# Kernel optimization log

Hardware: AMD Instinct MI355X
Metric: run time of the kernel (lower is better)

## Reference

```python
import jax, jax.numpy as jnp
import numpy as np

N_NODES = 100000
N_EDGES = 1600000
NFEAT, NHID, NCLASS = 64, 128, 32


def _glorot(key, shape):
    fan_in, fan_out = shape[0], shape[1]
    lim = np.sqrt(6.0 / (fan_in + fan_out))
    return jax.random.uniform(key, shape, jnp.float32, -lim, lim)


def setup_inputs() -> dict:
    key = jax.random.key(0)
    ks = jax.random.split(key, 12)
    x = jax.random.normal(ks[0], (N_NODES, NFEAT), jnp.float32)
    edge_idx = jax.random.randint(ks[1], (2, N_EDGES), 0, N_NODES, jnp.int64)
    edge_weight = jax.random.uniform(ks[2], (N_EDGES,), jnp.float32)
    return {
        "x": x,
        "edge_idx": edge_idx,
        "edge_weight": edge_weight,
        # SAGEConv 1: out = mean_agg(x) @ Wl1 + b1 + x @ Wr1
        "Wl1": _glorot(ks[3], (NFEAT, NHID)),
        "Wr1": _glorot(ks[4], (NFEAT, NHID)),
        "b1": jnp.zeros((NHID,), jnp.float32),
        # SAGEConv 2
        "Wl2": _glorot(ks[5], (NHID, NHID)),
        "Wr2": _glorot(ks[6], (NHID, NHID)),
        "b2": jnp.zeros((NHID,), jnp.float32),
        # fc head: Linear(nhid, nclass) -> Linear(nclass, 1)
        "Wfc1": _glorot(ks[7], (NHID, NCLASS)),
        "bfc1": jnp.zeros((NCLASS,), jnp.float32),
        "Wfc2": _glorot(ks[8], (NCLASS, 1)),
        "bfc2": jnp.zeros((1,), jnp.float32),
    }


def _sage_conv(x, src, dst, Wl, Wr, b, n_nodes):
    # mean aggregation of source features at destination nodes
    msg_sum = jax.ops.segment_sum(x[src], dst, num_segments=n_nodes)  # [N, d]
    deg = jax.ops.segment_sum(jnp.ones((src.shape[0], 1), x.dtype), dst,
                              num_segments=n_nodes)                    # [N, 1]
    mean = msg_sum / jnp.maximum(deg, 1.0)
    return mean @ Wl + b + x @ Wr


def reference(x, edge_idx, edge_weight, Wl1, Wr1, b1, Wl2, Wr2, b2,
              Wfc1, bfc1, Wfc2, bfc2):
    n_nodes = x.shape[0]
    src, dst = edge_idx[0], edge_idx[1]
    # dropout is identity in eval mode (training=False)
    h = _sage_conv(x, src, dst, Wl1, Wr1, b1, n_nodes)   # [N, nhid]
    h = _sage_conv(h, src, dst, Wl2, Wr2, b2, n_nodes)   # [N, nhid]
    h = h @ Wfc1 + bfc1                                   # [N, nclass]
    out = h @ Wfc2 + bfc2                                 # [N, 1]
    return out
```

## Files before the change

kernel.cpp:

```cpp
#include <hip/hip_runtime.h>

#define S_SHIFT 8
#define S_NODES 256
#define NBKT    400
#define CAP     5120
#define CHUNK   8192
#define NREP    4
#define FTH     512
#define NDOTS   160

__global__ __launch_bounds__(FTH) void fused_kernel(
    const float* __restrict__ x,
    const int* __restrict__ src, const int* __restrict__ dst,
    int E, int N, int B, int nscat,
    int* __restrict__ cursor, unsigned* __restrict__ bucket,
    const float* __restrict__ Wl1, const float* __restrict__ Wr1, const float* __restrict__ b1,
    const float* __restrict__ Wl2, const float* __restrict__ Wr2, const float* __restrict__ b2,
    const float* __restrict__ Wfc1, const float* __restrict__ bfc1,
    const float* __restrict__ Wfc2, const float* __restrict__ bfc2,
    float* __restrict__ ga, float2* __restrict__ gbc, float* __restrict__ c01)
{
    __shared__ int hist[NBKT], lbase[NBKT], lcur[NBKT];
    __shared__ float wv[192], uu[128], vl2[128], vr2[128], w2[32];
    int t = threadIdx.x;
    int l = t & 63;
    int w = t >> 6;

    if ((int)blockIdx.x < nscat) {
        int e0 = blockIdx.x * CHUNK;
        int cnt = E - e0; if (cnt > CHUNK) cnt = CHUNK;
        for (int i = t; i < B; i += FTH) hist[i] = 0;
        __syncthreads();
        for (int i = t; i < cnt; i += FTH)
            atomicAdd(&hist[dst[e0 + i] >> S_SHIFT], 1);
        __syncthreads();
        for (int i = t; i < B; i += FTH) {
            lcur[i] = 0;
            if (hist[i] > 0) lbase[i] = atomicAdd(&cursor[i], hist[i]);
        }
        __syncthreads();
        for (int i = t; i < cnt; i += FTH) {
            int d = dst[e0 + i], s = src[e0 + i];
            int bb = d >> S_SHIFT;
            int off = atomicAdd(&lcur[bb], 1);
            bucket[(size_t)bb * CAP + (unsigned)(lbase[bb] + off)] =
                ((unsigned)s << S_SHIFT) | (unsigned)(d & (S_NODES - 1));
        }
    } else {
        if (t < 32) w2[t] = Wfc2[t];
        __syncthreads();
        for (int j = 0; j < 16; ++j) {
            int i = w + 8 * j;
            float p = (l < 32) ? Wfc1[i * 32 + l] * w2[l] : 0.f;
            for (int m = 16; m; m >>= 1) p += __shfl_xor(p, m);
            if (l == 0) uu[i] = p;
        }
        __syncthreads();
        for (int j = 0; j < 16; ++j) {
            int i = w + 8 * j;
            float ua = uu[l], ub = uu[64 + l];
            float pa = Wl2[i * 128 + l] * ua + Wl2[i * 128 + 64 + l] * ub;
            float pb = Wr2[i * 128 + l] * ua + Wr2[i * 128 + 64 + l] * ub;
            for (int m = 32; m; m >>= 1) { pa += __shfl_xor(pa, m); pb += __shfl_xor(pb, m); }
            if (l == 0) { vl2[i] = pa; vr2[i] = pb; }
        }
        __syncthreads();
        for (int j = 0; j < 8; ++j) {
            int i = w + 8 * j;
            float l1a = Wl1[i * 128 + l], l1b = Wl1[i * 128 + 64 + l];
            float r1a = Wr1[i * 128 + l], r1b = Wr1[i * 128 + 64 + l];
            float La = vl2[l], Lb = vl2[64 + l], Ra = vr2[l], Rb = vr2[64 + l];
            float pc = l1a * La + l1b * Lb;
            float pb = l1a * Ra + l1b * Rb + r1a * La + r1b * Lb;
            float pa = r1a * Ra + r1b * Rb;
            for (int m = 32; m; m >>= 1) {
                pa += __shfl_xor(pa, m); pb += __shfl_xor(pb, m); pc += __shfl_xor(pc, m);
            }
            if (l == 0) { wv[i] = pa; wv[64 + i] = pb; wv[128 + i] = pc; }
        }
        if ((int)blockIdx.x == nscat && w == 7) {
            float p0 = b1[l] * vr2[l] + b1[64 + l] * vr2[64 + l]
                     + b2[l] * uu[l] + b2[64 + l] * uu[64 + l];
            if (l < 32) p0 += bfc1[l] * w2[l];
            float p1 = b1[l] * vl2[l] + b1[64 + l] * vl2[64 + l];
            for (int m = 32; m; m >>= 1) { p0 += __shfl_xor(p0, m); p1 += __shfl_xor(p1, m); }
            if (l == 0) { c01[0] = p0 + bfc2[0]; c01[1] = p1; }
        }
        __syncthreads();

        int fp = l & 15, sub = l >> 4;
        float4 wa4 = ((const float4*)wv)[fp];
        float4 wb4 = ((const float4*)wv)[16 + fp];
        float4 wc4 = ((const float4*)wv)[32 + fp];
        const float4* x4 = (const float4*)x;
        int Q = (N + 3) >> 2;
        for (int qd = ((int)blockIdx.x - nscat) * 8 + w; qd < Q; qd += NDOTS * 8) {
            int node = qd * 4 + sub;
            float a = 0.f, b = 0.f, c = 0.f;
            if (node < N) {
                float4 v = x4[(size_t)node * 16 + fp];
                a = v.x * wa4.x + v.y * wa4.y + v.z * wa4.z + v.w * wa4.w;
                b = v.x * wb4.x + v.y * wb4.y + v.z * wb4.z + v.w * wb4.w;
                c = v.x * wc4.x + v.y * wc4.y + v.z * wc4.z + v.w * wc4.w;
            }
            for (int m = 8; m; m >>= 1) {
                a += __shfl_xor(a, m); b += __shfl_xor(b, m); c += __shfl_xor(c, m);
            }
            if (fp == 0 && node < N) { ga[node] = a; gbc[node] = make_float2(b, c); }
        }
    }
}

__global__ __launch_bounds__(512) void aggA_kernel(
    const unsigned* __restrict__ bucket, const int* __restrict__ cursor,
    const float2* __restrict__ gbc, const float* __restrict__ ga,
    const float* __restrict__ c01,
    float* __restrict__ q, float* __restrict__ t1, float* __restrict__ inv, int N)
{
    __shared__ float aB[NREP][S_NODES], aC[NREP][S_NODES];
    __shared__ int cnt[NREP][S_NODES];
    int t = threadIdx.x, b = blockIdx.x;
    int r = (t >> 6) & (NREP - 1);
    float* aBf = (float*)aB; float* aCf = (float*)aC; int* cnf = (int*)cnt;
    for (int i = t; i < NREP * S_NODES; i += 512) { aBf[i] = 0.f; aCf[i] = 0.f; cnf[i] = 0; }
    __syncthreads();
    int n = cursor[b];
    const unsigned* bp = bucket + (size_t)b * CAP;
    for (int i = t; i < n; i += 512) {
        unsigned uu = bp[i];
        float2 g = gbc[uu >> S_SHIFT];
        int dl = uu & (S_NODES - 1);
        atomicAdd(&aB[r][dl], g.x);
        atomicAdd(&aC[r][dl], g.y);
        atomicAdd(&cnt[r][dl], 1);
    }
    __syncthreads();
    if (t < S_NODES) {
        int node = (b << S_SHIFT) + t;
        if (node < N) {
            float sb = aB[0][t] + aB[1][t] + aB[2][t] + aB[3][t];
            float sc = aC[0][t] + aC[1][t] + aC[2][t] + aC[3][t];
            int d = cnt[0][t] + cnt[1][t] + cnt[2][t] + cnt[3][t];
            float iv = 1.0f / ((d > 0) ? (float)d : 1.0f);
            inv[node] = iv;
            q[node]   = iv * sc;
            t1[node]  = ga[node] + iv * sb + c01[0] + (d > 0 ? c01[1] : 0.f);
        }
    }
}

__global__ __launch_bounds__(512) void aggB_kernel(
    const unsigned* __restrict__ bucket, const int* __restrict__ cursor,
    const float* __restrict__ q, const float* __restrict__ t1,
    const float* __restrict__ inv, float* __restrict__ out, int N)
{
    __shared__ float a2[NREP][S_NODES];
    int t = threadIdx.x, b = blockIdx.x;
    int r = (t >> 6) & (NREP - 1);
    float* a2f = (float*)a2;
    for (int i = t; i < NREP * S_NODES; i += 512) a2f[i] = 0.f;
    __syncthreads();
    int n = cursor[b];
    const unsigned* bp = bucket + (size_t)b * CAP;
    for (int i = t; i < n; i += 512) {
        unsigned uu = bp[i];
        atomicAdd(&a2[r][uu & (S_NODES - 1)], q[uu >> S_SHIFT]);
    }
    __syncthreads();
    if (t < S_NODES) {
        int node = (b << S_SHIFT) + t;
        if (node < N)
            out[node] = t1[node] + inv[node] * (a2[0][t] + a2[1][t] + a2[2][t] + a2[3][t]);
    }
}

extern "C" void kernel_launch(void* const* d_in, const int* in_sizes, int n_in,
                              void* d_out, int out_size, void* d_ws, size_t ws_size,
                              hipStream_t stream) {
    const float* x    = (const float*)d_in[0];
    const int*   eidx = (const int*)d_in[1];
    const float* Wl1  = (const float*)d_in[3];
    const float* Wr1  = (const float*)d_in[4];
    const float* b1   = (const float*)d_in[5];
    const float* Wl2  = (const float*)d_in[6];
    const float* Wr2  = (const float*)d_in[7];
    const float* b2   = (const float*)d_in[8];
    const float* Wfc1 = (const float*)d_in[9];
    const float* bfc1 = (const float*)d_in[10];
    const float* Wfc2 = (const float*)d_in[11];
    const float* bfc2 = (const float*)d_in[12];

    const int N = in_sizes[0] / 64;
    const int E = in_sizes[2];
    const int* src = eidx;
    const int* dst = eidx + E;
    const int B = (N + S_NODES - 1) / S_NODES;
    const int nscat = (E + CHUNK - 1) / CHUNK;

    char* ws = (char*)d_ws;
    int*      cursor = (int*)(ws);
    float*    c01    = (float*)(ws + 2048);
    float*    ga     = (float*)(ws + 4096);
    float*    q      = (float*)(ws + 4096 + (size_t)N * 4);
    float*    t1     = (float*)(ws + 4096 + (size_t)N * 8);
    float*    inv    = (float*)(ws + 4096 + (size_t)N * 12);
    float2*   gbc    = (float2*)(ws + 4096 + (size_t)N * 16);
    unsigned* bucket = (unsigned*)(ws + 4096 + (size_t)N * 24);

    hipMemsetAsync(cursor, 0, 2048, stream);

    fused_kernel<<<nscat + NDOTS, FTH, 0, stream>>>(
        x, src, dst, E, N, B, nscat, cursor, bucket,
        Wl1, Wr1, b1, Wl2, Wr2, b2, Wfc1, bfc1, Wfc2, bfc2,
        ga, gbc, c01);

    aggA_kernel<<<B, 512, 0, stream>>>(bucket, cursor, gbc, ga, c01, q, t1, inv, N);
    aggB_kernel<<<B, 512, 0, stream>>>(bucket, cursor, q, t1, inv, (float*)d_out, N);
}
```

Measured before the change: 171.1 us.

## Merge scatter and dot-product roles into uniform blocks with register-cached edges

The prep kernel no longer splits its blocks into edge-scatter blocks and node dot-product blocks. Every block now folds the weight matrices, scatters a smaller chunk of edges, then handles a grid-strided share of the per-node dot products. Edge src/dst values are loaded once into registers and reused between the histogram pass and the scatter pass, so they are not read from global memory twice. In exchange, every block repeats the small weight-folding work, and the halved chunk size means more global cursor atomics and more blocks.

```diff
diff --git a/kernel.cpp b/kernel.cpp
--- a/kernel.cpp
+++ b/kernel.cpp
@@ -4,15 +4,14 @@
 #define S_NODES 256
 #define NBKT    400
 #define CAP     5120
-#define CHUNK   8192
+#define CHUNK   4096
+#define EPT     8
 #define NREP    4
-#define FTH     512
-#define NDOTS   160
-
-__global__ __launch_bounds__(FTH) void fused_kernel(
+
+__global__ __launch_bounds__(512) void prep_kernel(
     const float* __restrict__ x,
     const int* __restrict__ src, const int* __restrict__ dst,
-    int E, int N, int B, int nscat,
+    int E, int N, int B,
     int* __restrict__ cursor, unsigned* __restrict__ bucket,
     const float* __restrict__ Wl1, const float* __restrict__ Wr1, const float* __restrict__ b1,
     const float* __restrict__ Wl2, const float* __restrict__ Wr2, const float* __restrict__ b2,
@@ -26,75 +25,86 @@
     int l = t & 63;
     int w = t >> 6;
 
-    if ((int)blockIdx.x < nscat) {
+    if (t < 32) w2[t] = Wfc2[t];
+    __syncthreads();
+    for (int j = 0; j < 16; ++j) {
+        int i = w + 8 * j;
+        float p = (l < 32) ? Wfc1[i * 32 + l] * w2[l] : 0.f;
+        for (int m = 16; m; m >>= 1) p += __shfl_xor(p, m);
+        if (l == 0) uu[i] = p;
+    }
+    __syncthreads();
+    for (int j = 0; j < 16; ++j) {
+        int i = w + 8 * j;
+        float ua = uu[l], ub = uu[64 + l];
+        float pa = Wl2[i * 128 + l] * ua + Wl2[i * 128 + 64 + l] * ub;
+        float pb = Wr2[i * 128 + l] * ua + Wr2[i * 128 + 64 + l] * ub;
+        for (int m = 32; m; m >>= 1) { pa += __shfl_xor(pa, m); pb += __shfl_xor(pb, m); }
+        if (l == 0) { vl2[i] = pa; vr2[i] = pb; }
+    }
+    __syncthreads();
+    for (int j = 0; j < 8; ++j) {
+        int i = w + 8 * j;
+        float l1a = Wl1[i * 128 + l], l1b = Wl1[i * 128 + 64 + l];
+        float r1a = Wr1[i * 128 + l], r1b = Wr1[i * 128 + 64 + l];
+        float La = vl2[l], Lb = vl2[64 + l], Ra = vr2[l], Rb = vr2[64 + l];
+        float pc = l1a * La + l1b * Lb;
+        float pb = l1a * Ra + l1b * Rb + r1a * La + r1b * Lb;
+        float pa = r1a * Ra + r1b * Rb;
+        for (int m = 32; m; m >>= 1) {
+            pa += __shfl_xor(pa, m); pb += __shfl_xor(pb, m); pc += __shfl_xor(pc, m);
+        }
+        if (l == 0) { wv[i] = pa; wv[64 + i] = pb; wv[128 + i] = pc; }
+    }
+    if (blockIdx.x == 0 && w == 7) {
+        float p0 = b1[l] * vr2[l] + b1[64 + l] * vr2[64 + l]
+                 + b2[l] * uu[l] + b2[64 + l] * uu[64 + l];
+        if (l < 32) p0 += bfc1[l] * w2[l];
+        float p1 = b1[l] * vl2[l] + b1[64 + l] * vl2[64 + l];
+        for (int m = 32; m; m >>= 1) { p0 += __shfl_xor(p0, m); p1 += __shfl_xor(p1, m); }
+        if (l == 0) { c01[0] = p0 + bfc2[0]; c01[1] = p1; }
+    }
+
+    {
         int e0 = blockIdx.x * CHUNK;
         int cnt = E - e0; if (cnt > CHUNK) cnt = CHUNK;
-        for (int i = t; i < B; i += FTH) hist[i] = 0;
+        int sd[EPT], ss[EPT];
+        for (int i = t; i < B; i += 512) hist[i] = 0;
         __syncthreads();
-        for (int i = t; i < cnt; i += FTH)
-            atomicAdd(&hist[dst[e0 + i] >> S_SHIFT], 1);
+        for (int k = 0; k < EPT; ++k) {
+            int i = t + k * 512;
+            if (i < cnt) {
+                sd[k] = dst[e0 + i];
+                ss[k] = src[e0 + i];
+                atomicAdd(&hist[sd[k] >> S_SHIFT], 1);
+            }
+        }
         __syncthreads();
-        for (int i = t; i < B; i += FTH) {
+        for (int i = t; i < B; i += 512) {
             lcur[i] = 0;
             if (hist[i] > 0) lbase[i] = atomicAdd(&cursor[i], hist[i]);
         }
         __syncthreads();
-        for (int i = t; i < cnt; i += FTH) {
-            int d = dst[e0 + i], s = src[e0 + i];
-            int bb = d >> S_SHIFT;
-            int off = atomicAdd(&lcur[bb], 1);
-            bucket[(size_t)bb * CAP + (unsigned)(lbase[bb] + off)] =
-                ((unsigned)s << S_SHIFT) | (unsigned)(d & (S_NODES - 1));
-        }
-    } else {
-        if (t < 32) w2[t] = Wfc2[t];
-        __syncthreads();
-        for (int j = 0; j < 16; ++j) {
-            int i = w + 8 * j;
-            float p = (l < 32) ? Wfc1[i * 32 + l] * w2[l] : 0.f;
-            for (int m = 16; m; m >>= 1) p += __shfl_xor(p, m);
-            if (l == 0) uu[i] = p;
-        }
-        __syncthreads();
-        for (int j = 0; j < 16; ++j) {
-            int i = w + 8 * j;
-            float ua = uu[l], ub = uu[64 + l];
-            float pa = Wl2[i * 128 + l] * ua + Wl2[i * 128 + 64 + l] * ub;
-            float pb = Wr2[i * 128 + l] * ua + Wr2[i * 128 + 64 + l] * ub;
-            for (int m = 32; m; m >>= 1) { pa += __shfl_xor(pa, m); pb += __shfl_xor(pb, m); }
-            if (l == 0) { vl2[i] = pa; vr2[i] = pb; }
-        }
-        __syncthreads();
-        for (int j = 0; j < 8; ++j) {
-            int i = w + 8 * j;
-            float l1a = Wl1[i * 128 + l], l1b = Wl1[i * 128 + 64 + l];
-            float r1a = Wr1[i * 128 + l], r1b = Wr1[i * 128 + 64 + l];
-            float La = vl2[l], Lb = vl2[64 + l], Ra = vr2[l], Rb = vr2[64 + l];
-            float pc = l1a * La + l1b * Lb;
-            float pb = l1a * Ra + l1b * Rb + r1a * La + r1b * Lb;
-            float pa = r1a * Ra + r1b * Rb;
-            for (int m = 32; m; m >>= 1) {
-                pa += __shfl_xor(pa, m); pb += __shfl_xor(pb, m); pc += __shfl_xor(pc, m);
-            }
-            if (l == 0) { wv[i] = pa; wv[64 + i] = pb; wv[128 + i] = pc; }
-        }
-        if ((int)blockIdx.x == nscat && w == 7) {
-            float p0 = b1[l] * vr2[l] + b1[64 + l] * vr2[64 + l]
-                     + b2[l] * uu[l] + b2[64 + l] * uu[64 + l];
-            if (l < 32) p0 += bfc1[l] * w2[l];
-            float p1 = b1[l] * vl2[l] + b1[64 + l] * vl2[64 + l];
-            for (int m = 32; m; m >>= 1) { p0 += __shfl_xor(p0, m); p1 += __shfl_xor(p1, m); }
-            if (l == 0) { c01[0] = p0 + bfc2[0]; c01[1] = p1; }
-        }
-        __syncthreads();
-
+        for (int k = 0; k < EPT; ++k) {
+            int i = t + k * 512;
+            if (i < cnt) {
+                int bb = sd[k] >> S_SHIFT;
+                int off = atomicAdd(&lcur[bb], 1);
+                bucket[(size_t)bb * CAP + (unsigned)(lbase[bb] + off)] =
+                    ((unsigned)ss[k] << S_SHIFT) | (unsigned)(sd[k] & (S_NODES - 1));
+            }
+        }
+    }
+
+    {
         int fp = l & 15, sub = l >> 4;
         float4 wa4 = ((const float4*)wv)[fp];
         float4 wb4 = ((const float4*)wv)[16 + fp];
         float4 wc4 = ((const float4*)wv)[32 + fp];
         const float4* x4 = (const float4*)x;
         int Q = (N + 3) >> 2;
-        for (int qd = ((int)blockIdx.x - nscat) * 8 + w; qd < Q; qd += NDOTS * 8) {
+        int stride = gridDim.x * 8;
+        for (int qd = blockIdx.x * 8 + w; qd < Q; qd += stride) {
             int node = qd * 4 + sub;
             float a = 0.f, b = 0.f, c = 0.f;
             if (node < N) {
@@ -195,7 +205,7 @@
     const int* src = eidx;
     const int* dst = eidx + E;
     const int B = (N + S_NODES - 1) / S_NODES;
-    const int nscat = (E + CHUNK - 1) / CHUNK;
+    const int nprep = (E + CHUNK - 1) / CHUNK;
 
     char* ws = (char*)d_ws;
     int*      cursor = (int*)(ws);
@@ -209,8 +219,8 @@
 
     hipMemsetAsync(cursor, 0, 2048, stream);
 
-    fused_kernel<<<nscat + NDOTS, FTH, 0, stream>>>(
-        x, src, dst, E, N, B, nscat, cursor, bucket,
+    prep_kernel<<<nprep, 512, 0, stream>>>(
+        x, src, dst, E, N, B, cursor, bucket,
         Wl1, Wr1, b1, Wl2, Wr2, b2, Wfc1, bfc1, Wfc2, bfc2,
         ga, gbc, c01);
 
```

After: 174.6 us. 2.1% more time.
